# Optimization experiments

Hardware: AMD Instinct MI355X
Metric: run time of the kernel (lower is better)

The kernel has to match this reference:

```python
import jax, jax.numpy as jnp
import numpy as np

BN_EPS = 1e-5


def setup_inputs() -> dict:
    key = jax.random.key(0)
    ks = jax.random.split(key, 4)
    N, V, C = 64, 512, 512
    K, OUT = 2, 512
    x = jax.random.normal(ks[0], (N, V, C), dtype=jnp.float32)
    A = jax.random.uniform(ks[1], (N, K, V, V), dtype=jnp.float32) / V
    conv_w = jax.random.normal(ks[2], (2 * OUT, C), dtype=jnp.float32) / np.sqrt(C)
    conv_b = jax.random.normal(ks[3], (2 * OUT,), dtype=jnp.float32) * 0.01
    gamma = jnp.ones((2 * OUT,), dtype=jnp.float32)
    beta = jnp.zeros((2 * OUT,), dtype=jnp.float32)
    eps_p = jnp.zeros((1,), dtype=jnp.float32)
    return {"x": x, "A": A, "conv_w": conv_w, "conv_b": conv_b,
            "gamma": gamma, "beta": beta, "eps_p": eps_p}


def reference(x, A, conv_w, conv_b, gamma, beta, eps_p):
    # x: (N, V, C); A: (N, K, V, V)
    N, V, C = x.shape
    K = A.shape[1]
    # 1x1 Conv1d over nodes: (N, 2*out, V)
    h = jnp.einsum('nvc,oc->nov', x, conv_w) + conv_b[None, :, None]
    # BatchNorm1d, training-mode batch stats (biased variance, per channel)
    mean = jnp.mean(h, axis=(0, 2), keepdims=True)
    var = jnp.var(h, axis=(0, 2), keepdims=True)
    h = (h - mean) * jax.lax.rsqrt(var + BN_EPS) * gamma[None, :, None] + beta[None, :, None]
    c2 = h.shape[1]
    h = h.reshape(N, K, c2 // K, V)  # (N, K, out, V)
    # graph propagation: x A then (x A) A^T, contracted over node dims
    t = jnp.einsum('nkcm,nkme->nkce', h, A)
    At = jnp.transpose(A, (0, 1, 3, 2))
    y = jnp.einsum('nkce,nkem->ncm', t, At)  # (N, out, V)
    out = (1.0 + eps_p[0]) * x + jnp.transpose(y, (0, 2, 1))
    return out, At
```

## Files before the change

kernel.cpp:

```cpp
#include <hip/hip_runtime.h>
#include <stdint.h>

typedef __bf16 bf16x8 __attribute__((ext_vector_type(8)));
typedef float f32x4 __attribute__((ext_vector_type(4)));
typedef unsigned short us4_t __attribute__((ext_vector_type(4)));
typedef unsigned short us8_t __attribute__((ext_vector_type(8)));

#define LDSK 40

__device__ __forceinline__ unsigned short f2bf(float f) {
  __bf16 b = (__bf16)f;
  return __builtin_bit_cast(unsigned short, b);
}
__device__ __forceinline__ float bf2f(unsigned short u) {
  union { uint32_t u; float f; } v; v.u = ((uint32_t)u) << 16;
  return v.f;
}

__device__ __forceinline__ void gload16(const unsigned short* g, unsigned short* l) {
  __builtin_amdgcn_global_load_lds(
      (const __attribute__((address_space(1))) void*)g,
      (__attribute__((address_space(3))) void*)l, 16, 0, 0);
}

__device__ __forceinline__ void stage_tile(const unsigned short* g, size_t ldg,
                                           unsigned short* lds, int wid, int lane) {
#pragma unroll
  for (int i = 0; i < 2; ++i) {
    int seg = wid * 2 + i;
    const unsigned short* gp = g + (size_t)(seg * 16 + (lane >> 2)) * ldg + (lane & 3) * 8;
    gload16(gp, lds + seg * 512);
  }
}

__global__ __launch_bounds__(256) void k_convert(
    const float* __restrict__ X, const float* __restrict__ W,
    unsigned short* __restrict__ Xb, unsigned short* __restrict__ Wb) {
  const size_t idx = (size_t)blockIdx.x * 256 + threadIdx.x;
  const size_t stride = (size_t)gridDim.x * 256;
  for (size_t i = idx; i < (size_t)16777216 / 8; i += stride) {
    float4 f0 = ((const float4*)X)[2 * i], f1 = ((const float4*)X)[2 * i + 1];
    us8_t w = { f2bf(f0.x), f2bf(f0.y), f2bf(f0.z), f2bf(f0.w),
                f2bf(f1.x), f2bf(f1.y), f2bf(f1.z), f2bf(f1.w) };
    ((us8_t*)Xb)[i] = w;
  }
  for (size_t i = idx; i < (size_t)524288 / 8; i += stride) {
    float4 f0 = ((const float4*)W)[2 * i], f1 = ((const float4*)W)[2 * i + 1];
    us8_t w = { f2bf(f0.x), f2bf(f0.y), f2bf(f0.z), f2bf(f0.w),
                f2bf(f1.x), f2bf(f1.y), f2bf(f1.z), f2bf(f1.w) };
    ((us8_t*)Wb)[i] = w;
  }
}

__global__ __launch_bounds__(256) void k_gemm1(
    const unsigned short* __restrict__ Wb, const unsigned short* __restrict__ Xb,
    const float* __restrict__ convb, unsigned short* __restrict__ H) {
  __shared__ unsigned short As[128][32];
  __shared__ unsigned short Bs[128][32];
  const int tid = threadIdx.x;
  const int L = blockIdx.x;
  const int xcd = L & 7, slot = L >> 3;
  const int n = xcd * 8 + (slot >> 5);
  const int tile = slot & 31;
  const int tm = tile >> 2, tn = tile & 3;
  const unsigned short* gA = Wb + (size_t)tm * 128 * 512;
  const unsigned short* gB = Xb + ((size_t)n * 512 + tn * 128) * 512;
  const int lane = tid & 63, wid = tid >> 6;
  const int wr = (wid >> 1) * 64, wc = (wid & 1) * 64;
  const int lr = lane & 15, lk = lane >> 4;
  f32x4 acc[4][4] = {};
  for (int k0 = 0; k0 < 512; k0 += 32) {
    stage_tile(gA + k0, 512, &As[0][0], wid, lane);
    stage_tile(gB + k0, 512, &Bs[0][0], wid, lane);
    __syncthreads();
    bf16x8 a[4], b[4];
#pragma unroll
    for (int mi = 0; mi < 4; ++mi) a[mi] = *(const bf16x8*)&As[wr + mi * 16 + lr][lk * 8];
#pragma unroll
    for (int ni = 0; ni < 4; ++ni) b[ni] = *(const bf16x8*)&Bs[wc + ni * 16 + lr][lk * 8];
#pragma unroll
    for (int mi = 0; mi < 4; ++mi)
#pragma unroll
      for (int ni = 0; ni < 4; ++ni)
        acc[mi][ni] = __builtin_amdgcn_mfma_f32_16x16x32_bf16(a[mi], b[ni], acc[mi][ni], 0, 0, 0);
    __syncthreads();
  }
  unsigned short* Hn = H + (size_t)n * 1024 * 512;
#pragma unroll
  for (int mi = 0; mi < 4; ++mi)
#pragma unroll
    for (int i = 0; i < 4; ++i) {
      int o = tm * 128 + wr + mi * 16 + lk * 4 + i;
      float bias = convb[o];
#pragma unroll
      for (int ni = 0; ni < 4; ++ni) {
        int v = tn * 128 + wc + ni * 16 + lr;
        Hn[(size_t)o * 512 + v] = f2bf(acc[mi][ni][i] + bias);
      }
    }
}

__global__ __launch_bounds__(256) void k_bn(
    const unsigned short* __restrict__ H, const float* __restrict__ gamma,
    const float* __restrict__ beta, float* __restrict__ sc_sh) {
  const int o = blockIdx.x;
  const int tid = threadIdx.x;
  const int g = tid >> 6, l = tid & 63;
  float s1 = 0.f, s2 = 0.f;
  for (int step = 0; step < 16; ++step) {
    int n = g + step * 4;
    const us8_t* row = (const us8_t*)(H + ((size_t)n * 1024 + o) * 512);
    us8_t v = row[l];
#pragma unroll
    for (int j = 0; j < 8; ++j) { float f = bf2f(v[j]); s1 += f; s2 += f * f; }
  }
  __shared__ float r1[256], r2[256];
  r1[tid] = s1; r2[tid] = s2;
  __syncthreads();
  for (int off = 128; off > 0; off >>= 1) {
    if (tid < off) { r1[tid] += r1[tid + off]; r2[tid] += r2[tid + off]; }
    __syncthreads();
  }
  if (tid == 0) {
    float mean = r1[0] * (1.0f / 32768.0f);
    float var = r2[0] * (1.0f / 32768.0f) - mean * mean;
    float s = gamma[o] * rsqrtf(var + 1e-5f);
    sc_sh[o] = s;
    sc_sh[1024 + o] = beta[o] - mean * s;
  }
}

__global__ __launch_bounds__(256) void k_affine(
    unsigned short* __restrict__ H, const float* __restrict__ sc_sh) {
  const size_t idx = (size_t)blockIdx.x * 256 + threadIdx.x;
  const size_t stride = (size_t)gridDim.x * 256;
  const size_t total8 = (size_t)64 * 1024 * 512 / 8;
  for (size_t i = idx; i < total8; i += stride) {
    size_t base = i * 8;
    int o = (int)((base >> 9) & 1023);
    float sc = sc_sh[o], sh = sc_sh[1024 + o];
    us8_t v = ((const us8_t*)H)[i];
    us8_t w;
#pragma unroll
    for (int j = 0; j < 8; ++j) w[j] = f2bf(fmaf(bf2f(v[j]), sc, sh));
    ((us8_t*)H)[i] = w;
  }
}

__global__ __launch_bounds__(256) void k_aat(
    const float* __restrict__ A, unsigned short* __restrict__ B2) {
  __shared__ unsigned short As[128][LDSK];
  __shared__ unsigned short Bs[128][LDSK];
  const int tid = threadIdx.x;
  const int L = blockIdx.x;
  const int xcd = L & 7, slot = L >> 3;
  const int nk = xcd * 16 + (slot >> 4);
  const int tile = slot & 15;
  const int tm = tile >> 2, tn = tile & 3;
  const float* Ank = A + (size_t)nk * 512 * 512;
  const float* gA = Ank + (size_t)tm * 128 * 512;
  const float* gB = Ank + (size_t)tn * 128 * 512;
  const int lane = tid & 63, wid = tid >> 6;
  const int wr = (wid >> 1) * 64, wc = (wid & 1) * 64;
  const int lr = lane & 15, lk = lane >> 4;
  f32x4 acc[4][4] = {};
  for (int k0 = 0; k0 < 512; k0 += 32) {
#pragma unroll
    for (int i = 0; i < 4; ++i) {
      int s = tid + i * 256;
      int r = s >> 3, c4 = (s & 7) * 4;
      float4 fa = *(const float4*)(gA + (size_t)r * 512 + k0 + c4);
      us4_t ua = { f2bf(fa.x), f2bf(fa.y), f2bf(fa.z), f2bf(fa.w) };
      *(us4_t*)&As[r][c4] = ua;
      float4 fb = *(const float4*)(gB + (size_t)r * 512 + k0 + c4);
      us4_t ub = { f2bf(fb.x), f2bf(fb.y), f2bf(fb.z), f2bf(fb.w) };
      *(us4_t*)&Bs[r][c4] = ub;
    }
    __syncthreads();
    bf16x8 a[4], b[4];
#pragma unroll
    for (int mi = 0; mi < 4; ++mi) a[mi] = *(const bf16x8*)&As[wr + mi * 16 + lr][lk * 8];
#pragma unroll
    for (int ni = 0; ni < 4; ++ni) b[ni] = *(const bf16x8*)&Bs[wc + ni * 16 + lr][lk * 8];
#pragma unroll
    for (int mi = 0; mi < 4; ++mi)
#pragma unroll
      for (int ni = 0; ni < 4; ++ni)
        acc[mi][ni] = __builtin_amdgcn_mfma_f32_16x16x32_bf16(a[mi], b[ni], acc[mi][ni], 0, 0, 0);
    __syncthreads();
  }
  unsigned short* Bn = B2 + (size_t)nk * 512 * 512;
#pragma unroll
  for (int mi = 0; mi < 4; ++mi)
#pragma unroll
    for (int i = 0; i < 4; ++i) {
      int m = tm * 128 + wr + mi * 16 + lk * 4 + i;
#pragma unroll
      for (int ni = 0; ni < 4; ++ni) {
        int mp = tn * 128 + wc + ni * 16 + lr;
        Bn[(size_t)m * 512 + mp] = f2bf(acc[mi][ni][i]);
      }
    }
}

template <bool AFFINE>
__global__ __launch_bounds__(256) void k_gemm3(
    const unsigned short* __restrict__ B2, const unsigned short* __restrict__ H,
    const float* __restrict__ sc_sh, const float* __restrict__ X,
    const float* __restrict__ epsp, float* __restrict__ out) {
  __shared__ unsigned short As[128][32];
  __shared__ unsigned short Bs[128][LDSK];
  __shared__ float s_sc[2][128], s_sh[2][128];
  const int tid = threadIdx.x;
  const int L = blockIdx.x;
  const int xcd = L & 7, slot = L >> 3;
  const int n = xcd * 8 + (slot >> 4);
  const int tile = slot & 15;
  const int tm = tile >> 2, tn = tile & 3;
  const int lane = tid & 63, wid = tid >> 6;
  const int wr = (wid >> 1) * 64, wc = (wid & 1) * 64;
  const int lr = lane & 15, lk = lane >> 4;
  if (AFFINE) {
    if (tid < 256) {
      int kkq = tid >> 7, r = tid & 127;
      s_sc[kkq][r] = sc_sh[kkq * 512 + tn * 128 + r];
      s_sh[kkq][r] = sc_sh[1024 + kkq * 512 + tn * 128 + r];
    }
    __syncthreads();
  }
  f32x4 acc[4][4] = {};
  for (int kk = 0; kk < 2; ++kk) {
    const unsigned short* gA = B2 + ((size_t)(n * 2 + kk) * 512 + tm * 128) * 512;
    const unsigned short* gB = H + ((size_t)n * 1024 + kk * 512 + tn * 128) * 512;
    for (int k0 = 0; k0 < 512; k0 += 32) {
      stage_tile(gA + k0, 512, &As[0][0], wid, lane);
#pragma unroll
      for (int i = 0; i < 2; ++i) {
        int s = tid + i * 256;
        int r = s >> 2, c8 = (s & 3) * 8;
        us8_t v = *(const us8_t*)(gB + (size_t)r * 512 + k0 + c8);
        if (AFFINE) {
          float sc = s_sc[kk][r], sh = s_sh[kk][r];
          us8_t w;
#pragma unroll
          for (int j = 0; j < 8; ++j) w[j] = f2bf(fmaf(bf2f(v[j]), sc, sh));
          *(us8_t*)&Bs[r][c8] = w;
        } else {
          *(us8_t*)&Bs[r][c8] = v;
        }
      }
      __syncthreads();
      bf16x8 a[4], b[4];
#pragma unroll
      for (int mi = 0; mi < 4; ++mi) a[mi] = *(const bf16x8*)&As[wr + mi * 16 + lr][lk * 8];
#pragma unroll
      for (int ni = 0; ni < 4; ++ni) b[ni] = *(const bf16x8*)&Bs[wc + ni * 16 + lr][lk * 8];
#pragma unroll
      for (int mi = 0; mi < 4; ++mi)
#pragma unroll
        for (int ni = 0; ni < 4; ++ni)
          acc[mi][ni] = __builtin_amdgcn_mfma_f32_16x16x32_bf16(a[mi], b[ni], acc[mi][ni], 0, 0, 0);
      __syncthreads();
    }
  }
  const float e1 = 1.0f + epsp[0];
#pragma unroll
  for (int mi = 0; mi < 4; ++mi)
#pragma unroll
    for (int i = 0; i < 4; ++i) {
      int v = tm * 128 + wr + mi * 16 + lk * 4 + i;
#pragma unroll
      for (int ni = 0; ni < 4; ++ni) {
        int c = tn * 128 + wc + ni * 16 + lr;
        size_t idx = ((size_t)n * 512 + v) * 512 + c;
        out[idx] = fmaf(e1, X[idx], acc[mi][ni][i]);
      }
    }
}

__global__ void k_at(const float* __restrict__ A, float* __restrict__ At) {
  __shared__ float tile[32][33];
  const int nk = blockIdx.z;
  const int e0 = blockIdx.x * 32, m0 = blockIdx.y * 32;
  const float* src = A + (size_t)nk * 512 * 512;
  float* dst = At + (size_t)nk * 512 * 512;
  const int tx = threadIdx.x, ty = threadIdx.y;
#pragma unroll
  for (int yy = ty; yy < 32; yy += 8)
    tile[yy][tx] = src[(size_t)(m0 + yy) * 512 + e0 + tx];
  __syncthreads();
#pragma unroll
  for (int yy = ty; yy < 32; yy += 8)
    dst[(size_t)(e0 + yy) * 512 + m0 + tx] = tile[tx][yy];
}

extern "C" void kernel_launch(void* const* d_in, const int* in_sizes, int n_in,
                              void* d_out, int out_size, void* d_ws, size_t ws_size,
                              hipStream_t stream) {
  const float* x      = (const float*)d_in[0];
  const float* A      = (const float*)d_in[1];
  const float* conv_w = (const float*)d_in[2];
  const float* conv_b = (const float*)d_in[3];
  const float* gamma  = (const float*)d_in[4];
  const float* beta   = (const float*)d_in[5];
  const float* eps_p  = (const float*)d_in[6];

  float* out = (float*)d_out;
  float* At  = out + (size_t)16777216;

  unsigned short* B2 = (unsigned short*)At;
  unsigned short* H  = (unsigned short*)(At + (size_t)16777216);
  unsigned short* Xb = (unsigned short*)out;
  unsigned short* Wb = Xb + (size_t)16777216;

  const bool use_ws = (ws_size >= 8192);
  float* sc_sh = use_ws ? (float*)d_ws : out;

  k_convert<<<2048, 256, 0, stream>>>(x, conv_w, Xb, Wb);
  k_gemm1  <<<2048, 256, 0, stream>>>(Wb, Xb, conv_b, H);
  k_bn     <<<1024, 256, 0, stream>>>(H, gamma, beta, sc_sh);
  k_aat    <<<2048, 256, 0, stream>>>(A, B2);
  if (use_ws) {
    k_gemm3<true><<<1024, 256, 0, stream>>>(B2, H, sc_sh, x, eps_p, out);
  } else {
    k_affine<<<2048, 256, 0, stream>>>(H, sc_sh);
    k_gemm3<false><<<1024, 256, 0, stream>>>(B2, H, nullptr, x, eps_p, out);
  }
  k_at<<<dim3(16, 16, 128), dim3(32, 8), 0, stream>>>(A, At);
}
```

Baseline: 316.3 us.

## Exploit symmetry of A·Aᵀ to compute only upper tiles, widen transpose tiles

```diff
diff --git a/kernel.cpp b/kernel.cpp
--- a/kernel.cpp
+++ b/kernel.cpp
@@ -149,14 +149,18 @@
 
 __global__ __launch_bounds__(256) void k_aat(
     const float* __restrict__ A, unsigned short* __restrict__ B2) {
-  __shared__ unsigned short As[128][LDSK];
-  __shared__ unsigned short Bs[128][LDSK];
+  __shared__ unsigned short smem[2 * 128 * LDSK];
+  unsigned short (*As)[LDSK] = (unsigned short(*)[LDSK])smem;
+  unsigned short (*Bs)[LDSK] = (unsigned short(*)[LDSK])(smem + 128 * LDSK);
   const int tid = threadIdx.x;
   const int L = blockIdx.x;
   const int xcd = L & 7, slot = L >> 3;
-  const int nk = xcd * 16 + (slot >> 4);
-  const int tile = slot & 15;
-  const int tm = tile >> 2, tn = tile & 3;
+  const int nk = xcd * 16 + slot / 10;
+  const int t = slot % 10;
+  const int tm = (t >= 4) + (t >= 7) + (t >= 9);
+  const int base = (tm == 0) ? 0 : (tm == 1) ? 4 : (tm == 2) ? 7 : 9;
+  const int tn = t - base + tm;
+  const bool diag = (tm == tn);
   const float* Ank = A + (size_t)nk * 512 * 512;
   const float* gA = Ank + (size_t)tm * 128 * 512;
   const float* gB = Ank + (size_t)tn * 128 * 512;
@@ -172,16 +176,23 @@
       float4 fa = *(const float4*)(gA + (size_t)r * 512 + k0 + c4);
       us4_t ua = { f2bf(fa.x), f2bf(fa.y), f2bf(fa.z), f2bf(fa.w) };
       *(us4_t*)&As[r][c4] = ua;
-      float4 fb = *(const float4*)(gB + (size_t)r * 512 + k0 + c4);
-      us4_t ub = { f2bf(fb.x), f2bf(fb.y), f2bf(fb.z), f2bf(fb.w) };
-      *(us4_t*)&Bs[r][c4] = ub;
+      if (!diag) {
+        float4 fb = *(const float4*)(gB + (size_t)r * 512 + k0 + c4);
+        us4_t ub = { f2bf(fb.x), f2bf(fb.y), f2bf(fb.z), f2bf(fb.w) };
+        *(us4_t*)&Bs[r][c4] = ub;
+      }
     }
     __syncthreads();
     bf16x8 a[4], b[4];
 #pragma unroll
     for (int mi = 0; mi < 4; ++mi) a[mi] = *(const bf16x8*)&As[wr + mi * 16 + lr][lk * 8];
-#pragma unroll
-    for (int ni = 0; ni < 4; ++ni) b[ni] = *(const bf16x8*)&Bs[wc + ni * 16 + lr][lk * 8];
+    if (diag) {
+#pragma unroll
+      for (int ni = 0; ni < 4; ++ni) b[ni] = *(const bf16x8*)&As[wc + ni * 16 + lr][lk * 8];
+    } else {
+#pragma unroll
+      for (int ni = 0; ni < 4; ++ni) b[ni] = *(const bf16x8*)&Bs[wc + ni * 16 + lr][lk * 8];
+    }
 #pragma unroll
     for (int mi = 0; mi < 4; ++mi)
 #pragma unroll
@@ -201,6 +212,35 @@
         Bn[(size_t)m * 512 + mp] = f2bf(acc[mi][ni][i]);
       }
     }
+  if (!diag) {
+    unsigned short (*Tl)[136] = (unsigned short(*)[136])smem;
+#pragma unroll
+    for (int h = 0; h < 2; ++h) {
+      __syncthreads();
+      if ((wid & 1) == h) {
+#pragma unroll
+        for (int ni = 0; ni < 4; ++ni)
+#pragma unroll
+          for (int mi = 0; mi < 4; ++mi)
+#pragma unroll
+            for (int i = 0; i < 4; i += 2) {
+              int rloc = ni * 16 + lr;
+              int cloc = wr + mi * 16 + lk * 4 + i;
+              uint32_t pair = (uint32_t)f2bf(acc[mi][ni][i]) |
+                              ((uint32_t)f2bf(acc[mi][ni][i + 1]) << 16);
+              *(uint32_t*)&Tl[rloc][cloc] = pair;
+            }
+      }
+      __syncthreads();
+#pragma unroll
+      for (int j = 0; j < 4; ++j) {
+        int ch = tid + j * 256;
+        int r = ch >> 4, c8 = (ch & 15) * 8;
+        us8_t v = *(const us8_t*)&Tl[r][c8];
+        *(us8_t*)&Bn[(size_t)(tn * 128 + h * 64 + r) * 512 + tm * 128 + c8] = v;
+      }
+    }
+  }
 }
 
 template <bool AFFINE>
@@ -278,20 +318,29 @@
     }
 }
 
-__global__ void k_at(const float* __restrict__ A, float* __restrict__ At) {
-  __shared__ float tile[32][33];
+__global__ __launch_bounds__(256) void k_at(
+    const float* __restrict__ A, float* __restrict__ At) {
+  __shared__ float tile[64][65];
   const int nk = blockIdx.z;
-  const int e0 = blockIdx.x * 32, m0 = blockIdx.y * 32;
-  const float* src = A + (size_t)nk * 512 * 512;
-  float* dst = At + (size_t)nk * 512 * 512;
-  const int tx = threadIdx.x, ty = threadIdx.y;
-#pragma unroll
-  for (int yy = ty; yy < 32; yy += 8)
-    tile[yy][tx] = src[(size_t)(m0 + yy) * 512 + e0 + tx];
+  const int e0 = blockIdx.x * 64, m0 = blockIdx.y * 64;
+  const float* src = A + (size_t)nk * 262144;
+  float* dst = At + (size_t)nk * 262144;
+  const int t = threadIdx.x;
+#pragma unroll
+  for (int j = 0; j < 4; ++j) {
+    int ch = t + j * 256;
+    int r = ch >> 4, c4 = (ch & 15) * 4;
+    float4 f = *(const float4*)(src + (size_t)(m0 + r) * 512 + e0 + c4);
+    tile[r][c4] = f.x; tile[r][c4 + 1] = f.y; tile[r][c4 + 2] = f.z; tile[r][c4 + 3] = f.w;
+  }
   __syncthreads();
 #pragma unroll
-  for (int yy = ty; yy < 32; yy += 8)
-    dst[(size_t)(e0 + yy) * 512 + m0 + tx] = tile[tx][yy];
+  for (int j = 0; j < 4; ++j) {
+    int ch = t + j * 256;
+    int e = ch >> 4, m4 = (ch & 15) * 4;
+    float4 g = { tile[m4][e], tile[m4 + 1][e], tile[m4 + 2][e], tile[m4 + 3][e] };
+    *(float4*)(dst + (size_t)(e0 + e) * 512 + m0 + m4) = g;
+  }
 }
 
 extern "C" void kernel_launch(void* const* d_in, const int* in_sizes, int n_in,
@@ -319,12 +368,12 @@
   k_convert<<<2048, 256, 0, stream>>>(x, conv_w, Xb, Wb);
   k_gemm1  <<<2048, 256, 0, stream>>>(Wb, Xb, conv_b, H);
   k_bn     <<<1024, 256, 0, stream>>>(H, gamma, beta, sc_sh);
-  k_aat    <<<2048, 256, 0, stream>>>(A, B2);
+  k_aat    <<<1280, 256, 0, stream>>>(A, B2);
   if (use_ws) {
     k_gemm3<true><<<1024, 256, 0, stream>>>(B2, H, sc_sh, x, eps_p, out);
   } else {
     k_affine<<<2048, 256, 0, stream>>>(H, sc_sh);
     k_gemm3<false><<<1024, 256, 0, stream>>>(B2, H, nullptr, x, eps_p, out);
   }
-  k_at<<<dim3(16, 16, 128), dim3(32, 8), 0, stream>>>(A, At);
-}
+  k_at<<<dim3(8, 8, 128), 256, 0, stream>>>(A, At);
+}
```

Result: slower. 328.3 us (+3.8%).
